# Optimization experiments

Hardware: AMD Instinct MI355X
Metric: run time of the kernel (lower is better)

The kernel has to match this reference:

```python
import jax, jax.numpy as jnp
import numpy as np


def conv3x3(x, w):
    # x: [B,C,H,W], w: [O,I,3,3], stride 1, pad 1, no bias
    return jax.lax.conv_general_dilated(
        x, w, window_strides=(1, 1), padding=[(1, 1), (1, 1)],
        dimension_numbers=("NCHW", "OIHW", "NCHW"))


def deform_conv2d(x, offset, w):
    """torchvision-style DeformConv2d: k=3, stride=1, pad=1, dilation=1,
    1 offset group, no bias. x:[B,C,H,W], offset:[B,18,H,W] (dy,dx pairs
    per kernel tap, k = kh*3+kw), w:[O,C,3,3]. Zero padding outside."""
    B, C, H, W = x.shape
    K = 9
    dy = offset[:, 0::2]  # [B,9,H,W]
    dx = offset[:, 1::2]
    kh = (jnp.arange(K) // 3 - 1).astype(x.dtype)[None, :, None, None]
    kw = (jnp.arange(K) % 3 - 1).astype(x.dtype)[None, :, None, None]
    hh = jnp.arange(H, dtype=x.dtype)[None, None, :, None]
    ww = jnp.arange(W, dtype=x.dtype)[None, None, None, :]
    py = hh + kh + dy  # sampling y coord, [B,9,H,W]
    px = ww + kw + dx
    y0 = jnp.floor(py)
    x0 = jnp.floor(px)
    wy = py - y0
    wx = px - x0
    x_hwc = jnp.transpose(x, (0, 2, 3, 1))  # [B,H,W,C]
    b_idx = jnp.arange(B)[:, None, None, None]

    def gather(yi, xi):
        valid = (yi >= 0) & (yi <= H - 1) & (xi >= 0) & (xi <= W - 1)
        yc = jnp.clip(yi, 0, H - 1).astype(jnp.int32)
        xc = jnp.clip(xi, 0, W - 1).astype(jnp.int32)
        v = x_hwc[b_idx, yc, xc]  # [B,9,H,W,C]
        return v * valid[..., None].astype(x.dtype)

    v00 = gather(y0, x0)
    v01 = gather(y0, x0 + 1)
    v10 = gather(y0 + 1, x0)
    v11 = gather(y0 + 1, x0 + 1)
    wy = wy[..., None]
    wx = wx[..., None]
    sampled = (v00 * (1 - wy) * (1 - wx) + v01 * (1 - wy) * wx
               + v10 * wy * (1 - wx) + v11 * wy * wx)  # [B,9,H,W,C]
    wk = w.reshape(w.shape[0], w.shape[1], K)  # [O,C,9]
    return jnp.einsum("bkhwc,ock->bohw", sampled, wk)


def setup_inputs() -> dict:
    key = jax.random.key(0)
    ks = jax.random.split(key, 6)
    B, C, H, W = 2, 128, 128, 128
    s = 0.05  # small init so learned offsets stay in a realistic range
    return {
        "input_features": jax.random.normal(ks[0], (B, C, H, W), jnp.float32),
        "reference_features": jax.random.normal(ks[1], (B, C, H, W), jnp.float32),
        "w_est1": jax.random.normal(ks[2], (C, 2 * C, 3, 3), jnp.float32) * s,
        "w_est2": jax.random.normal(ks[3], (C, C, 3, 3), jnp.float32) * s,
        "w_off": jax.random.normal(ks[4], (18, C, 3, 3), jnp.float32) * s,
        "w_def": jax.random.normal(ks[5], (C, C, 3, 3), jnp.float32) * s,
    }


def reference(input_features, reference_features, w_est1, w_est2, w_off, w_def):
    # concat input+reference features along channel dim
    feat = jnp.concatenate([input_features, reference_features], axis=1)  # [B,2C,H,W]
    # dynamic offset estimator: 2-layer 3x3 conv stack 2C->C->C with ReLU
    est = jax.nn.relu(conv3x3(feat, w_est1))
    est = jax.nn.relu(conv3x3(est, w_est2))
    # offset head: C -> 2*9 offsets per pixel
    offset = conv3x3(est, w_off)  # [B,18,H,W]
    # deformable conv over the reference features
    return deform_conv2d(reference_features, offset, w_def)
```

## Files before the change

### kernel.cpp

```cpp
#include <hip/hip_runtime.h>

typedef _Float16 f16;
typedef __attribute__((ext_vector_type(8))) _Float16 f16x8;
typedef __attribute__((ext_vector_type(4))) float f32x4;


__device__ __forceinline__ void g2l16(const void* g, void* l) {
  __builtin_amdgcn_global_load_lds((const __attribute__((address_space(1))) void*)g,
                                   (__attribute__((address_space(3))) void*)l, 16, 0, 0);
}

__device__ __forceinline__ void pack_conv(const float* __restrict__ src, f16* __restrict__ dst,
                                          long idx, int C) {
  int ci3 = idx & 7;
  int g = (idx >> 3) & 3;
  long t = idx >> 5;
  int o = (int)(t & 63); t >>= 6;
  int kx = (int)(t % 3); t /= 3;
  int nb = (int)(t & 1); t >>= 1;
  int nkc = C >> 5;
  int cc = (int)(t % nkc);
  int ky = (int)(t / nkc);
  int og = nb * 64 + o;
  int c = (cc << 5) + ((g ^ ((o >> 1) & 3)) << 3) + ci3;
  dst[idx] = (f16)src[(((size_t)og * C + c) * 3 + ky) * 3 + kx];
}

__device__ __forceinline__ void halo_zero(f16* __restrict__ buf, long e) {
  int c = (int)(e & 127);
  long t = e >> 7;
  int b = (int)(t / 516);
  int p = (int)(t % 516);
  int y, x;
  if (p < 130)      { y = 0;   x = p; }
  else if (p < 260) { y = 129; x = p - 130; }
  else if (p < 388) { x = 0;   y = p - 259; }
  else              { x = 129; y = p - 387; }
  buf[((size_t)(b * 130 + y) * 130 + x) * 128 + c] = (f16)0.f;
}

__global__ __launch_bounds__(256) void init_k(const float* __restrict__ x, const float* __restrict__ ref,
                                              const float* __restrict__ w1, const float* __restrict__ w2,
                                              const float* __restrict__ woff, const float* __restrict__ wdef,
                                              f16* __restrict__ W1p, f16* __restrict__ W2p,
                                              f16* __restrict__ Woffp, f16* __restrict__ Wdefp,
                                              f16* __restrict__ xP, f16* __restrict__ refP,
                                              f16* __restrict__ est1, f16* __restrict__ est2) {
  __shared__ __align__(16) f16 T[64][40];
  int tid = threadIdx.x;
  if (blockIdx.x < 4096) {
    int bi = blockIdx.x;
    int row = bi & 255, wseg = (bi >> 8) & 1, chunk = bi >> 9;
    int b = row >> 7, h = row & 127;
    int w0 = wseg * 64;
    const float* src = (chunk < 4) ? x : ref;
    f16* dstp = (chunk < 4) ? xP : refP;
    int c0 = (chunk & 3) * 32;
#pragma unroll
    for (int i = 0; i < 2; ++i) {
      int idx = tid + i * 256;
      int c = idx >> 4, g = idx & 15;
      const float4 v = *(const float4*)(src + (((size_t)(b * 128 + c0 + c)) * 128 + h) * 128 + w0 + g * 4);
      T[g * 4 + 0][c] = (f16)v.x;
      T[g * 4 + 1][c] = (f16)v.y;
      T[g * 4 + 2][c] = (f16)v.z;
      T[g * 4 + 3][c] = (f16)v.w;
    }
    __syncthreads();
    int w = tid >> 2, g = tid & 3;
    f16x8 o = *(const f16x8*)&T[w][g * 8];
    *(f16x8*)(dstp + ((size_t)(b * 130 + h + 1) * 130 + w0 + w + 1) * 128 + c0 + g * 8) = o;
    return;
  }
  long idx = (long)(blockIdx.x - 4096) * 256 + tid;
  if (idx < 294912) { pack_conv(w1, W1p, idx, 256); return; }
  idx -= 294912;
  if (idx < 147456) { pack_conv(w2, W2p, idx, 128); return; }
  idx -= 147456;
  if (idx < 36864) {
    int ci3 = (int)(idx & 7);
    int g = (int)((idx >> 3) & 3);
    int o = (int)((idx >> 5) & 31);
    int t2 = (int)(idx >> 10);
    int kx = t2 % 3; t2 /= 3;
    int cc = t2 & 3, ky = t2 >> 2;
    int c = (cc << 5) + ((g ^ ((o >> 1) & 3)) << 3) + ci3;
    Woffp[idx] = (o < 18) ? (f16)woff[(((size_t)o * 128 + c) * 3 + ky) * 3 + kx] : (f16)0.f;
    return;
  }
  idx -= 36864;
  if (idx < 147456) {
    int j = (int)(idx & 7);
    int ln = (int)((idx >> 3) & 63);
    int ofr = (int)((idx >> 9) & 7);
    int cc = (int)((idx >> 12) & 3);
    int t = (int)(idx >> 14);
    int o = ofr * 16 + (ln & 15);
    int c = cc * 32 + (ln >> 4) * 8 + j;
    Wdefp[idx] = (f16)wdef[(((size_t)o * 128 + c) * 3 + t / 3) * 3 + t % 3];
    return;
  }
  idx -= 147456;
  if (idx < 132096) { halo_zero(xP, idx); return; }
  idx -= 132096;
  if (idx < 132096) { halo_zero(refP, idx); return; }
  idx -= 132096;
  if (idx < 132096) { halo_zero(est1, idx); return; }
  idx -= 132096;
  if (idx < 132096) halo_zero(est2, idx);
}

template <int NKC>
__global__ __launch_bounds__(256, 3) void conv_k(const f16* __restrict__ src0,
                                                 const f16* __restrict__ src1,
                                                 const f16* __restrict__ Wp,
                                                 f16* __restrict__ dst) {
  constexpr int S = 3 * NKC;
  const int j = blockIdx.x;
  const int xcd = j & 7, ji = j >> 3;
  const int row = xcd * 32 + (ji & 31);
  const int nb = ji >> 5;
  const int b = row >> 7, h = row & 127;
  __shared__ __align__(16) f16 As[2][130][32];
  __shared__ __align__(16) f16 Bs[2][3][64][32];
  const int tid = threadIdx.x;
  const int lane = tid & 63, wave = tid >> 6;
  const int l16 = lane & 15, quad = lane >> 4;
  const int wmB = wave * 32;
  f32x4 acc[2][4] = {};

  auto stage = [&](int s, int buf) {
    int ky = s / NKC, cc = s % NKC;
    const f16* sp = (NKC == 8 && cc >= 4) ? src1 : src0;
    int c0 = (NKC == 8 ? (cc & 3) : cc) * 32;
    const f16* abase = sp + ((size_t)(b * 130 + h + ky) * 130) * 128 + c0;
#pragma unroll
    for (int rr = 0; rr < 2; ++rr) {
      int ch = rr * 256 + tid;
      int xx = ch >> 2, g = ch & 3;
      g2l16(abase + (size_t)xx * 128 + ((g ^ ((xx >> 1) & 3)) << 3),
            (char*)&As[buf][0][0] + ch * 16);
    }
    if (tid < 8) {
      int ch = 512 + tid;
      int xx = ch >> 2, g = ch & 3;
      g2l16(abase + (size_t)xx * 128 + ((g ^ ((xx >> 1) & 3)) << 3),
            (char*)&As[buf][0][0] + ch * 16);
    }
    const f16* bbase = Wp + (size_t)((ky * NKC + cc) * 2 + nb) * (3 * 64 * 32);
#pragma unroll
    for (int rr = 0; rr < 3; ++rr) {
      int ch = rr * 256 + tid;
      g2l16(bbase + (size_t)ch * 8, (char*)&Bs[buf][0][0][0] + ch * 16);
    }
  };

  stage(0, 0);
  __syncthreads();
  for (int s = 0; s < S; ++s) {
    if (s + 1 < S) stage(s + 1, (s + 1) & 1);
    const int buf = s & 1;
#pragma unroll
    for (int kx = 0; kx < 3; ++kx) {
      f16x8 bf[4];
#pragma unroll
      for (int j2 = 0; j2 < 4; ++j2) {
        int o = j2 * 16 + l16;
        bf[j2] = *(const f16x8*)&Bs[buf][kx][o][(quad ^ ((o >> 1) & 3)) << 3];
      }
#pragma unroll
      for (int i = 0; i < 2; ++i) {
        int xx = wmB + i * 16 + l16 + kx;
        f16x8 a = *(const f16x8*)&As[buf][xx][(quad ^ ((xx >> 1) & 3)) << 3];
#pragma unroll
        for (int j2 = 0; j2 < 4; ++j2)
          acc[i][j2] = __builtin_amdgcn_mfma_f32_16x16x32_f16(a, bf[j2], acc[i][j2], 0, 0, 0);
      }
    }
    __syncthreads();
  }
#pragma unroll
  for (int i = 0; i < 2; ++i)
#pragma unroll
    for (int j2 = 0; j2 < 4; ++j2) {
      int o = nb * 64 + j2 * 16 + l16;
#pragma unroll
      for (int rr = 0; rr < 4; ++rr) {
        int m = wmB + i * 16 + quad * 4 + rr;
        float v = fmaxf(acc[i][j2][rr], 0.f);
        dst[((size_t)(b * 130 + h + 1) * 130 + m + 1) * 128 + o] = (f16)v;
      }
    }
}

__global__ __launch_bounds__(256, 3) void conv_off_k(const f16* __restrict__ src,
                                                     const f16* __restrict__ Wp,
                                                     float* __restrict__ dst) {
  const int j = blockIdx.x;
  const int row = (j & 7) * 32 + (j >> 3);
  const int b = row >> 7, h = row & 127;
  __shared__ __align__(16) f16 As[2][130][32];
  __shared__ __align__(16) f16 Bs[2][3][32][32];
  const int tid = threadIdx.x;
  const int lane = tid & 63, wave = tid >> 6;
  const int l16 = lane & 15, quad = lane >> 4;
  const int wmB = wave * 32;
  f32x4 acc[2][2] = {};

  auto stage = [&](int s, int buf) {
    int ky = s >> 2, cc = s & 3;
    const f16* abase = src + ((size_t)(b * 130 + h + ky) * 130) * 128 + cc * 32;
#pragma unroll
    for (int rr = 0; rr < 2; ++rr) {
      int ch = rr * 256 + tid;
      int xx = ch >> 2, g = ch & 3;
      g2l16(abase + (size_t)xx * 128 + ((g ^ ((xx >> 1) & 3)) << 3),
            (char*)&As[buf][0][0] + ch * 16);
    }
    if (tid < 8) {
      int ch = 512 + tid;
      int xx = ch >> 2, g = ch & 3;
      g2l16(abase + (size_t)xx * 128 + ((g ^ ((xx >> 1) & 3)) << 3),
            (char*)&As[buf][0][0] + ch * 16);
    }
    const f16* bbase = Wp + (size_t)(ky * 4 + cc) * (3 * 32 * 32);
    {
      g2l16(bbase + (size_t)tid * 8, (char*)&Bs[buf][0][0][0] + tid * 16);
      if (tid < 128) {
        int ch = 256 + tid;
        g2l16(bbase + (size_t)ch * 8, (char*)&Bs[buf][0][0][0] + ch * 16);
      }
    }
  };

  stage(0, 0);
  __syncthreads();
  for (int s = 0; s < 12; ++s) {
    if (s + 1 < 12) stage(s + 1, (s + 1) & 1);
    const int buf = s & 1;
#pragma unroll
    for (int kx = 0; kx < 3; ++kx) {
      f16x8 bf[2];
#pragma unroll
      for (int j2 = 0; j2 < 2; ++j2) {
        int o = j2 * 16 + l16;
        bf[j2] = *(const f16x8*)&Bs[buf][kx][o][(quad ^ ((o >> 1) & 3)) << 3];
      }
#pragma unroll
      for (int i = 0; i < 2; ++i) {
        int xx = wmB + i * 16 + l16 + kx;
        f16x8 a = *(const f16x8*)&As[buf][xx][(quad ^ ((xx >> 1) & 3)) << 3];
#pragma unroll
        for (int j2 = 0; j2 < 2; ++j2)
          acc[i][j2] = __builtin_amdgcn_mfma_f32_16x16x32_f16(a, bf[j2], acc[i][j2], 0, 0, 0);
      }
    }
    __syncthreads();
  }
#pragma unroll
  for (int i = 0; i < 2; ++i)
#pragma unroll
    for (int j2 = 0; j2 < 2; ++j2)
#pragma unroll
      for (int rr = 0; rr < 4; ++rr) {
        int m = wmB + i * 16 + quad * 4 + rr;
        int o = j2 * 16 + l16;
        dst[((size_t)row * 128 + m) * 32 + o] = acc[i][j2][rr];
      }
}

__global__ __launch_bounds__(256, 3) void deform_k(const f16* __restrict__ refP,
                                                   const float* __restrict__ offb,
                                                   const f16* __restrict__ Wdefp,
                                                   float* __restrict__ out) {
  const int j = blockIdx.x;
  const int xcd = j & 7, ji = j >> 3;
  const int row = xcd * 32 + (ji & 31);
  const int tile = ji >> 5;
  const int b = row >> 7, h = row & 127;
  __shared__ __align__(16) f16 Ss[2][64][128];
  __shared__ int4 meta[9][64];
  const int tid = threadIdx.x;
  const int lane = tid & 63, wave = tid >> 6;
  const int l16 = lane & 15, quad = lane >> 4;

  for (int e = tid; e < 576; e += 256) {
    int t = e >> 6, p = e & 63;
    int wg = tile * 64 + p;
    const float2 d = *(const float2*)(offb + ((size_t)row * 128 + wg) * 32 + 2 * t);
    float py = (float)(h + t / 3 - 1) + d.x;
    float px = (float)(wg + t % 3 - 1) + d.y;
    float fy = floorf(py), fx = floorf(px);
    meta[t][p] = make_int4((int)fy, (int)fx, __float_as_int(py - fy), __float_as_int(px - fx));
  }

  auto sample = [&](int t, int buf) {
    const int p = tid >> 2, cg = tid & 3;
    int4 mt = meta[t][p];
    int yp = mt.x + 1, xp = mt.y + 1;
    float wy = __int_as_float(mt.z), wx = __int_as_float(mt.w);
    bool y0v = (unsigned)yp < 130u, y1v = (unsigned)(yp + 1) < 130u;
    bool x0v = (unsigned)xp < 130u, x1v = (unsigned)(xp + 1) < 130u;
    int cy0 = y0v ? yp : 0, cy1 = y1v ? yp + 1 : 0;
    int cx0 = x0v ? xp : 0, cx1 = x1v ? xp + 1 : 0;
    float u0 = (1.f - wy) * (y0v ? 1.f : 0.f), u1 = wy * (y1v ? 1.f : 0.f);
    float s0 = (1.f - wx) * (x0v ? 1.f : 0.f), s1 = wx * (x1v ? 1.f : 0.f);
    f16 h00 = (f16)(u0 * s0), h01 = (f16)(u0 * s1);
    f16 h10 = (f16)(u1 * s0), h11 = (f16)(u1 * s1);
    const size_t bb = (size_t)b * 130;
    const f16* p00 = refP + ((bb + cy0) * 130 + cx0) * 128 + cg * 32;
    const f16* p01 = refP + ((bb + cy0) * 130 + cx1) * 128 + cg * 32;
    const f16* p10 = refP + ((bb + cy1) * 130 + cx0) * 128 + cg * 32;
    const f16* p11 = refP + ((bb + cy1) * 130 + cx1) * 128 + cg * 32;
    f16x8 v00[4], v01[4], v10[4], v11[4];
#pragma unroll
    for (int q = 0; q < 4; ++q) {
      v00[q] = *(const f16x8*)(p00 + q * 8);
      v01[q] = *(const f16x8*)(p01 + q * 8);
      v10[q] = *(const f16x8*)(p10 + q * 8);
      v11[q] = *(const f16x8*)(p11 + q * 8);
    }
#pragma unroll
    for (int q = 0; q < 4; ++q) {
      f16x8 rb = v00[q] * h00 + v01[q] * h01 + v10[q] * h10 + v11[q] * h11;
      int c = cg * 4 + q;
      *(f16x8*)&Ss[buf][p][(c ^ (p & 7)) << 3] = rb;
    }
  };

  f32x4 acc[2][4] = {};
  __syncthreads();
  sample(0, 0);
  __syncthreads();
  for (int t = 0; t < 9; ++t) {
    f16x8 af[4][2];
#pragma unroll
    for (int cc = 0; cc < 4; ++cc)
#pragma unroll
      for (int i = 0; i < 2; ++i)
        af[cc][i] = *(const f16x8*)(Wdefp +
            ((((size_t)t * 4 + cc) * 8 + wave * 2 + i) * 64 + lane) * 8);
    if (t < 8) sample(t + 1, (t + 1) & 1);
    const int buf = t & 1;
#pragma unroll
    for (int cc = 0; cc < 4; ++cc) {
      f16x8 bf[4];
#pragma unroll
      for (int j2 = 0; j2 < 4; ++j2) {
        int p = j2 * 16 + l16;
        bf[j2] = *(const f16x8*)&Ss[buf][p][((cc * 4 + quad) ^ (p & 7)) << 3];
      }
#pragma unroll
      for (int i = 0; i < 2; ++i)
#pragma unroll
        for (int j2 = 0; j2 < 4; ++j2)
          acc[i][j2] = __builtin_amdgcn_mfma_f32_16x16x32_f16(af[cc][i], bf[j2], acc[i][j2], 0, 0, 0);
    }
    __syncthreads();
  }
#pragma unroll
  for (int i = 0; i < 2; ++i)
#pragma unroll
    for (int rr = 0; rr < 4; ++rr) {
      int o = wave * 32 + i * 16 + quad * 4 + rr;
#pragma unroll
      for (int j2 = 0; j2 < 4; ++j2) {
        int wg = tile * 64 + j2 * 16 + l16;
        out[((size_t)(b * 128 + o) * 128 + h) * 128 + wg] = acc[i][j2][rr];
      }
    }
}

extern "C" void kernel_launch(void* const* d_in, const int* in_sizes, int n_in,
                              void* d_out, int out_size, void* d_ws, size_t ws_size,
                              hipStream_t stream) {
  const float* x = (const float*)d_in[0];
  const float* ref = (const float*)d_in[1];
  const float* w1 = (const float*)d_in[2];
  const float* w2 = (const float*)d_in[3];
  const float* woff = (const float*)d_in[4];
  const float* wdef = (const float*)d_in[5];
  float* out = (float*)d_out;
  char* ws = (char*)d_ws;
  f16* xP = (f16*)(ws + 0);
  f16* refP = (f16*)(ws + 8652800);
  f16* est1 = (f16*)(ws + 17305600);
  f16* est2 = (f16*)(ws + 25958400);
  float* offb = (float*)(ws + 34611200);
  f16* W1p = (f16*)(ws + 38805504);
  f16* W2p = (f16*)(ws + 39395328);
  f16* Woffp = (f16*)(ws + 39690240);
  f16* Wdefp = (f16*)(ws + 39763968);

  init_k<<<dim3(8608), 256, 0, stream>>>(x, ref, w1, w2, woff, wdef,
                                         W1p, W2p, Woffp, Wdefp, xP, refP, est1, est2);
  conv_k<8><<<dim3(512), 256, 0, stream>>>(xP, refP, W1p, est1);
  conv_k<4><<<dim3(512), 256, 0, stream>>>(est1, est1, W2p, est2);
  conv_off_k<<<dim3(256), 256, 0, stream>>>(est2, Woffp, offb);
  deform_k<<<dim3(512), 256, 0, stream>>>(refP, offb, Wdefp, out);
}
```

Baseline: 169.1 us.

## Switch conv and deform GEMMs to 32x32x16 MFMA with full-N tiles

The two 3x3 conv kernels now use 32x32x16 MFMA instructions. Each block computes all 128 output channels for one row instead of splitting N across two blocks, which halves the grid to 256 blocks and doubles the weight tile in LDS. The deform kernel also moves to 32x32x16 MFMA with a 2x2 wave split over output channels and pixels, and the weight packing and LDS swizzles are changed to match. This aims to raise MFMA throughput per LDS read and to drop the redundant A-tile loads. In exchange it uses more LDS and registers, lowers occupancy (launch bounds loosened), and launches fewer blocks across the CUs.

```diff
diff --git a/kernel.cpp b/kernel.cpp
--- a/kernel.cpp
+++ b/kernel.cpp
@@ -3,6 +3,7 @@
 typedef _Float16 f16;
 typedef __attribute__((ext_vector_type(8))) _Float16 f16x8;
 typedef __attribute__((ext_vector_type(4))) float f32x4;
+typedef __attribute__((ext_vector_type(16))) float f32x16;
 
 
 __device__ __forceinline__ void g2l16(const void* g, void* l) {
@@ -15,15 +16,13 @@
   int ci3 = idx & 7;
   int g = (idx >> 3) & 3;
   long t = idx >> 5;
-  int o = (int)(t & 63); t >>= 6;
+  int o = (int)(t & 127); t >>= 7;
   int kx = (int)(t % 3); t /= 3;
-  int nb = (int)(t & 1); t >>= 1;
   int nkc = C >> 5;
   int cc = (int)(t % nkc);
   int ky = (int)(t / nkc);
-  int og = nb * 64 + o;
-  int c = (cc << 5) + ((g ^ ((o >> 1) & 3)) << 3) + ci3;
-  dst[idx] = (f16)src[(((size_t)og * C + c) * 3 + ky) * 3 + kx];
+  int c = (cc << 5) + ((g ^ (o & 3)) << 3) + ci3;
+  dst[idx] = (f16)src[(((size_t)o * C + c) * 3 + ky) * 3 + kx];
 }
 
 __device__ __forceinline__ void halo_zero(f16* __restrict__ buf, long e) {
@@ -90,13 +89,14 @@
   }
   idx -= 36864;
   if (idx < 147456) {
-    int j = (int)(idx & 7);
+    int jj = (int)(idx & 7);
     int ln = (int)((idx >> 3) & 63);
-    int ofr = (int)((idx >> 9) & 7);
+    int oblk = (int)((idx >> 9) & 3);
+    int q = (int)((idx >> 11) & 1);
     int cc = (int)((idx >> 12) & 3);
     int t = (int)(idx >> 14);
-    int o = ofr * 16 + (ln & 15);
-    int c = cc * 32 + (ln >> 4) * 8 + j;
+    int o = oblk * 32 + (ln & 31);
+    int c = cc * 32 + q * 16 + (ln >> 5) * 8 + jj;
     Wdefp[idx] = (f16)wdef[(((size_t)o * 128 + c) * 3 + t / 3) * 3 + t % 3];
     return;
   }
@@ -111,23 +111,21 @@
 }
 
 template <int NKC>
-__global__ __launch_bounds__(256, 3) void conv_k(const f16* __restrict__ src0,
-                                                 const f16* __restrict__ src1,
-                                                 const f16* __restrict__ Wp,
-                                                 f16* __restrict__ dst) {
+__global__ __launch_bounds__(256) void conv_k(const f16* __restrict__ src0,
+                                              const f16* __restrict__ src1,
+                                              const f16* __restrict__ Wp,
+                                              f16* __restrict__ dst) {
   constexpr int S = 3 * NKC;
   const int j = blockIdx.x;
-  const int xcd = j & 7, ji = j >> 3;
-  const int row = xcd * 32 + (ji & 31);
-  const int nb = ji >> 5;
+  const int row = (j & 7) * 32 + (j >> 3);
   const int b = row >> 7, h = row & 127;
   __shared__ __align__(16) f16 As[2][130][32];
-  __shared__ __align__(16) f16 Bs[2][3][64][32];
+  __shared__ __align__(16) f16 Bs[2][3][128][32];
   const int tid = threadIdx.x;
   const int lane = tid & 63, wave = tid >> 6;
-  const int l16 = lane & 15, quad = lane >> 4;
-  const int wmB = wave * 32;
-  f32x4 acc[2][4] = {};
+  const int l31 = lane & 31, lh = lane >> 5;
+  const int wpx = (wave & 1) * 64, wn = (wave >> 1) * 64;
+  f32x16 acc[2][2] = {};
 
   auto stage = [&](int s, int buf) {
     int ky = s / NKC, cc = s % NKC;
@@ -138,18 +136,18 @@
     for (int rr = 0; rr < 2; ++rr) {
       int ch = rr * 256 + tid;
       int xx = ch >> 2, g = ch & 3;
-      g2l16(abase + (size_t)xx * 128 + ((g ^ ((xx >> 1) & 3)) << 3),
+      g2l16(abase + (size_t)xx * 128 + ((g ^ (xx & 3)) << 3),
             (char*)&As[buf][0][0] + ch * 16);
     }
     if (tid < 8) {
       int ch = 512 + tid;
       int xx = ch >> 2, g = ch & 3;
-      g2l16(abase + (size_t)xx * 128 + ((g ^ ((xx >> 1) & 3)) << 3),
+      g2l16(abase + (size_t)xx * 128 + ((g ^ (xx & 3)) << 3),
             (char*)&As[buf][0][0] + ch * 16);
     }
-    const f16* bbase = Wp + (size_t)((ky * NKC + cc) * 2 + nb) * (3 * 64 * 32);
-#pragma unroll
-    for (int rr = 0; rr < 3; ++rr) {
+    const f16* bbase = Wp + (size_t)(ky * NKC + cc) * (3 * 128 * 32);
+#pragma unroll
+    for (int rr = 0; rr < 6; ++rr) {
       int ch = rr * 256 + tid;
       g2l16(bbase + (size_t)ch * 8, (char*)&Bs[buf][0][0][0] + ch * 16);
     }
@@ -162,33 +160,43 @@
     const int buf = s & 1;
 #pragma unroll
     for (int kx = 0; kx < 3; ++kx) {
-      f16x8 bf[4];
-#pragma unroll
-      for (int j2 = 0; j2 < 4; ++j2) {
-        int o = j2 * 16 + l16;
-        bf[j2] = *(const f16x8*)&Bs[buf][kx][o][(quad ^ ((o >> 1) & 3)) << 3];
-      }
-#pragma unroll
-      for (int i = 0; i < 2; ++i) {
-        int xx = wmB + i * 16 + l16 + kx;
-        f16x8 a = *(const f16x8*)&As[buf][xx][(quad ^ ((xx >> 1) & 3)) << 3];
-#pragma unroll
-        for (int j2 = 0; j2 < 4; ++j2)
-          acc[i][j2] = __builtin_amdgcn_mfma_f32_16x16x32_f16(a, bf[j2], acc[i][j2], 0, 0, 0);
-      }
+      f16x8 af[2][2], bf[2][2];
+#pragma unroll
+      for (int mb = 0; mb < 2; ++mb)
+#pragma unroll
+        for (int q = 0; q < 2; ++q) {
+          int xx = wpx + mb * 32 + l31 + kx;
+          int c = q * 2 + lh;
+          af[mb][q] = *(const f16x8*)&As[buf][xx][(c ^ (xx & 3)) << 3];
+        }
+#pragma unroll
+      for (int nb = 0; nb < 2; ++nb)
+#pragma unroll
+        for (int q = 0; q < 2; ++q) {
+          int o = wn + nb * 32 + l31;
+          int c = q * 2 + lh;
+          bf[nb][q] = *(const f16x8*)&Bs[buf][kx][o][(c ^ (o & 3)) << 3];
+        }
+#pragma unroll
+      for (int mb = 0; mb < 2; ++mb)
+#pragma unroll
+        for (int nb = 0; nb < 2; ++nb)
+#pragma unroll
+          for (int q = 0; q < 2; ++q)
+            acc[mb][nb] = __builtin_amdgcn_mfma_f32_32x32x16_f16(af[mb][q], bf[nb][q], acc[mb][nb], 0, 0, 0);
     }
     __syncthreads();
   }
 #pragma unroll
-  for (int i = 0; i < 2; ++i)
-#pragma unroll
-    for (int j2 = 0; j2 < 4; ++j2) {
-      int o = nb * 64 + j2 * 16 + l16;
-#pragma unroll
-      for (int rr = 0; rr < 4; ++rr) {
-        int m = wmB + i * 16 + quad * 4 + rr;
-        float v = fmaxf(acc[i][j2][rr], 0.f);
-        dst[((size_t)(b * 130 + h + 1) * 130 + m + 1) * 128 + o] = (f16)v;
+  for (int mb = 0; mb < 2; ++mb)
+#pragma unroll
+    for (int nb = 0; nb < 2; ++nb) {
+      int o = wn + nb * 32 + l31;
+#pragma unroll
+      for (int reg = 0; reg < 16; ++reg) {
+        int px = wpx + mb * 32 + 4 * lh + (reg & 3) + 8 * (reg >> 2);
+        float v = fmaxf(acc[mb][nb][reg], 0.f);
+        dst[((size_t)(b * 130 + h + 1) * 130 + px + 1) * 128 + o] = (f16)v;
       }
     }
 }
@@ -269,7 +277,7 @@
       }
 }
 
-__global__ __launch_bounds__(256, 3) void deform_k(const f16* __restrict__ refP,
+__global__ __launch_bounds__(256, 2) void deform_k(const f16* __restrict__ refP,
                                                    const float* __restrict__ offb,
                                                    const f16* __restrict__ Wdefp,
                                                    float* __restrict__ out) {
@@ -282,7 +290,8 @@
   __shared__ int4 meta[9][64];
   const int tid = threadIdx.x;
   const int lane = tid & 63, wave = tid >> 6;
-  const int l16 = lane & 15, quad = lane >> 4;
+  const int l31 = lane & 31, lh = lane >> 5;
+  const int wo = wave >> 1, wp = wave & 1;
 
   for (int e = tid; e < 576; e += 256) {
     int t = e >> 6, p = e & 63;
@@ -328,47 +337,46 @@
     }
   };
 
-  f32x4 acc[2][4] = {};
+  f32x16 acc[2] = {};
   __syncthreads();
   sample(0, 0);
   __syncthreads();
   for (int t = 0; t < 9; ++t) {
-    f16x8 af[4][2];
+    f16x8 af[4][2][2];
 #pragma unroll
     for (int cc = 0; cc < 4; ++cc)
 #pragma unroll
-      for (int i = 0; i < 2; ++i)
-        af[cc][i] = *(const f16x8*)(Wdefp +
-            ((((size_t)t * 4 + cc) * 8 + wave * 2 + i) * 64 + lane) * 8);
+      for (int q = 0; q < 2; ++q)
+#pragma unroll
+        for (int mb = 0; mb < 2; ++mb) {
+          int oblk = wo * 2 + mb;
+          af[cc][q][mb] = *(const f16x8*)(Wdefp +
+              ((((size_t)(t * 4 + cc) * 2 + q) * 4 + oblk) * 64 + lane) * 8);
+        }
     if (t < 8) sample(t + 1, (t + 1) & 1);
     const int buf = t & 1;
 #pragma unroll
-    for (int cc = 0; cc < 4; ++cc) {
-      f16x8 bf[4];
-#pragma unroll
-      for (int j2 = 0; j2 < 4; ++j2) {
-        int p = j2 * 16 + l16;
-        bf[j2] = *(const f16x8*)&Ss[buf][p][((cc * 4 + quad) ^ (p & 7)) << 3];
-      }
-#pragma unroll
-      for (int i = 0; i < 2; ++i)
-#pragma unroll
-        for (int j2 = 0; j2 < 4; ++j2)
-          acc[i][j2] = __builtin_amdgcn_mfma_f32_16x16x32_f16(af[cc][i], bf[j2], acc[i][j2], 0, 0, 0);
-    }
+    for (int cc = 0; cc < 4; ++cc)
+#pragma unroll
+      for (int q = 0; q < 2; ++q) {
+        int c = cc * 4 + q * 2 + lh;
+        int p = wp * 32 + l31;
+        f16x8 bf = *(const f16x8*)&Ss[buf][p][(c ^ (p & 7)) << 3];
+#pragma unroll
+        for (int mb = 0; mb < 2; ++mb)
+          acc[mb] = __builtin_amdgcn_mfma_f32_32x32x16_f16(af[cc][q][mb], bf, acc[mb], 0, 0, 0);
+      }
     __syncthreads();
   }
 #pragma unroll
-  for (int i = 0; i < 2; ++i)
-#pragma unroll
-    for (int rr = 0; rr < 4; ++rr) {
-      int o = wave * 32 + i * 16 + quad * 4 + rr;
-#pragma unroll
-      for (int j2 = 0; j2 < 4; ++j2) {
-        int wg = tile * 64 + j2 * 16 + l16;
-        out[((size_t)(b * 128 + o) * 128 + h) * 128 + wg] = acc[i][j2][rr];
-      }
-    }
+  for (int mb = 0; mb < 2; ++mb) {
+    int px = tile * 64 + wp * 32 + l31;
+#pragma unroll
+    for (int reg = 0; reg < 16; ++reg) {
+      int o = wo * 64 + mb * 32 + 4 * lh + (reg & 3) + 8 * (reg >> 2);
+      out[((size_t)(b * 128 + o) * 128 + h) * 128 + px] = acc[mb][reg];
+    }
+  }
 }
 
 extern "C" void kernel_launch(void* const* d_in, const int* in_sizes, int n_in,
@@ -394,8 +402,8 @@
 
   init_k<<<dim3(8608), 256, 0, stream>>>(x, ref, w1, w2, woff, wdef,
                                          W1p, W2p, Woffp, Wdefp, xP, refP, est1, est2);
-  conv_k<8><<<dim3(512), 256, 0, stream>>>(xP, refP, W1p, est1);
-  conv_k<4><<<dim3(512), 256, 0, stream>>>(est1, est1, W2p, est2);
+  conv_k<8><<<dim3(256), 256, 0, stream>>>(xP, refP, W1p, est1);
+  conv_k<4><<<dim3(256), 256, 0, stream>>>(est1, est1, W2p, est2);
   conv_off_k<<<dim3(256), 256, 0, stream>>>(est2, Woffp, offb);
   deform_k<<<dim3(512), 256, 0, stream>>>(refP, offb, Wdefp, out);
 }
```

Result: slower. 196.2 us (+16.1%).
